# Kernel optimization log

Measured on AMD Instinct MI355X. Metric: run time of the kernel, lower is better.

Reference implementation:

```python
import jax, jax.numpy as jnp
import numpy as np

B, S, HID = 2, 2048, 3072
H, KV, D = 16, 8, 256
EPS = 1e-6
SCALE = D ** -0.5  # query_pre_attn_scalar is None -> head_dim**-0.5
NEG = -1e9


def setup_inputs() -> dict:
    key = jax.random.key(0)
    ks = jax.random.split(key, 7)
    hidden_states = jax.random.normal(ks[0], (B, S, HID), jnp.float32)
    # rotary tables: freqs_cis = exp(i * pos * theta_j), theta_j = 10000^(-2j/D)
    pos = jnp.arange(S, dtype=jnp.float32)
    inv_freq = 1.0 / (10000.0 ** (jnp.arange(0, D, 2, dtype=jnp.float32) / D))  # [D/2]
    ang = pos[:, None] * inv_freq[None, :]  # [S, D/2]
    freqs_cos = jnp.cos(ang)
    freqs_sin = jnp.sin(ang)
    # additive causal mask [1,1,S,S]
    causal = jnp.tril(jnp.ones((S, S), dtype=bool))
    mask = jnp.where(causal, 0.0, NEG).astype(jnp.float32)[None, None]
    q_w = jax.random.normal(ks[1], (HID, H * D), jnp.float32) * 0.02
    k_w = jax.random.normal(ks[2], (HID, KV * D), jnp.float32) * 0.02
    v_w = jax.random.normal(ks[3], (HID, KV * D), jnp.float32) * 0.02
    o_w = jax.random.normal(ks[4], (H * D, HID), jnp.float32) * 0.02
    qnorm_w = jax.random.normal(ks[5], (D,), jnp.float32) * 0.1
    knorm_w = jax.random.normal(ks[6], (D,), jnp.float32) * 0.1
    return dict(hidden_states=hidden_states, freqs_cos=freqs_cos, freqs_sin=freqs_sin,
                mask=mask, q_w=q_w, k_w=k_w, v_w=v_w, o_w=o_w,
                qnorm_w=qnorm_w, knorm_w=knorm_w)


def rmsnorm(x, w, eps=EPS):
    # RMSNorm with add_unit_offset: x * rsqrt(mean(x^2)+eps) * (1 + w)
    x32 = x.astype(jnp.float32)
    n = x32 * jax.lax.rsqrt(jnp.mean(x32 * x32, axis=-1, keepdims=True) + eps)
    return (n * (1.0 + w.astype(jnp.float32))).astype(x.dtype)


def rope(x, cos, sin):
    # x: [B, S, Hx, D]; complex mult with (x1 + i x2), then concat(real, imag)
    x1, x2 = jnp.split(x, 2, axis=-1)  # each [B,S,Hx,D/2]
    c = cos[None, :, None, :]
    s = sin[None, :, None, :]
    return jnp.concatenate([x1 * c - x2 * s, x1 * s + x2 * c], axis=-1)


def reference(hidden_states, freqs_cos, freqs_sin, mask, q_w, k_w, v_w, o_w, qnorm_w, knorm_w):
    bsz, seqlen = hidden_states.shape[0], hidden_states.shape[1]
    xq = (hidden_states @ q_w).reshape(bsz, seqlen, H, D)
    xk = (hidden_states @ k_w).reshape(bsz, seqlen, KV, D)
    xv = (hidden_states @ v_w).reshape(bsz, seqlen, KV, D)
    # QK-norm (use_qk_norm=True)
    xq = rmsnorm(xq, qnorm_w)
    xk = rmsnorm(xk, knorm_w)
    # rotary embeddings
    xq = rope(xq, freqs_cos, freqs_sin)
    xk = rope(xk, freqs_cos, freqs_sin)
    # GQA: repeat kv heads to match query heads
    rep = H // KV
    xk = jnp.repeat(xk, rep, axis=2)
    xv = jnp.repeat(xv, rep, axis=2)
    q = jnp.transpose(xq, (0, 2, 1, 3)) * SCALE  # [B,H,S,D]
    k = jnp.transpose(xk, (0, 2, 1, 3))
    v = jnp.transpose(xv, (0, 2, 1, 3))
    scores = jnp.einsum('bhqd,bhkd->bhqk', q, k) + mask
    probs = jax.nn.softmax(scores.astype(jnp.float32), axis=-1).astype(q.dtype)
    out = jnp.einsum('bhqk,bhkd->bhqd', probs, v)
    out = jnp.transpose(out, (0, 2, 1, 3)).reshape(bsz, seqlen, H * D)
    return out @ o_w
```

## Files before the change

kernel.cpp:

```cpp
#include <hip/hip_runtime.h>
#include <hip/hip_bf16.h>
#include <cstdint>

#define B_   2
#define S_   2048
#define HID_ 3072
#define H_   16
#define KV_  8
#define D_   256
#define HD_  4096
#define KVD_ 2048

constexpr float EPS_   = 1e-6f;
constexpr float SCALE_ = 0.0625f;

typedef unsigned short u16;
typedef __attribute__((ext_vector_type(8))) short bf16x8;
typedef __attribute__((ext_vector_type(4))) float f32x4;

__device__ inline float bf2f(u16 u) { return __uint_as_float(((unsigned int)u) << 16); }
__device__ inline u16 f2bf(float f) {
  unsigned int x = __float_as_uint(f);
  x += 0x7fffu + ((x >> 16) & 1u);
  return (u16)(x >> 16);
}

__device__ inline void gll16(const u16* g, u16* l) {
  __builtin_amdgcn_global_load_lds((const __attribute__((address_space(1))) unsigned int*)g,
                                   (__attribute__((address_space(3))) unsigned int*)l,
                                   16, 0, 0);
}

__global__ void cast_f32_bf16(const float* __restrict__ in, u16* __restrict__ out, int n4) {
  int i = blockIdx.x * blockDim.x + threadIdx.x;
  if (i < n4) {
    float4 v = ((const float4*)in)[i];
    ushort4 o;
    o.x = f2bf(v.x); o.y = f2bf(v.y); o.z = f2bf(v.z); o.w = f2bf(v.w);
    ((ushort4*)out)[i] = o;
  }
}

__global__ void transpose_cast(const float* __restrict__ in, u16* __restrict__ out, int K, int N) {
  __shared__ __align__(16) float tile[64][65];
  int n0 = blockIdx.x * 64, k0 = blockIdx.y * 64;
  int t = threadIdx.x;
  int rr = t >> 4, cc = (t & 15) * 4;
  for (int i = 0; i < 4; i++) {
    float4 v = *(const float4*)(&in[(size_t)(k0 + rr + 16 * i) * N + n0 + cc]);
    tile[rr + 16 * i][cc + 0] = v.x; tile[rr + 16 * i][cc + 1] = v.y;
    tile[rr + 16 * i][cc + 2] = v.z; tile[rr + 16 * i][cc + 3] = v.w;
  }
  __syncthreads();
  for (int i = 0; i < 4; i++) {
    int orow = rr + 16 * i;
    ushort4 o;
    o.x = f2bf(tile[cc + 0][orow]); o.y = f2bf(tile[cc + 1][orow]);
    o.z = f2bf(tile[cc + 2][orow]); o.w = f2bf(tile[cc + 3][orow]);
    *(ushort4*)(&out[(size_t)(n0 + orow) * K + k0 + cc]) = o;
  }
}

__global__ void transpose_v(const u16* __restrict__ in, u16* __restrict__ out) {
  __shared__ __align__(16) u16 tile[64][68];
  int n0 = blockIdx.x * 64, tk0 = blockIdx.y * 64;
  int b = tk0 >> 11, s0 = tk0 & (S_ - 1);
  int t = threadIdx.x;
  int rr = t >> 4, cc = (t & 15) * 4;
  for (int i = 0; i < 4; i++) {
    ushort4 v = *(const ushort4*)(&in[(size_t)(tk0 + rr + 16 * i) * KVD_ + n0 + cc]);
    tile[rr + 16 * i][cc + 0] = v.x; tile[rr + 16 * i][cc + 1] = v.y;
    tile[rr + 16 * i][cc + 2] = v.z; tile[rr + 16 * i][cc + 3] = v.w;
  }
  __syncthreads();
  for (int i = 0; i < 4; i++) {
    int orow = rr + 16 * i;
    ushort4 o;
    o.x = tile[cc + 0][orow]; o.y = tile[cc + 1][orow];
    o.z = tile[cc + 2][orow]; o.w = tile[cc + 3][orow];
    *(ushort4*)(&out[((size_t)b << 22) + (size_t)(n0 + orow) * S_ + s0 + cc]) = o;
  }
}

template <bool OUTF32>
__global__ __launch_bounds__(256) void gemm_bf16(const u16* __restrict__ A,
                                                 const u16* __restrict__ Bt,
                                                 void* __restrict__ Cv, int M, int N, int K) {
  __shared__ __align__(16) u16 As[128 * 32];
  __shared__ __align__(16) u16 Bs[128 * 32];
  int t = threadIdx.x, lane = t & 63, wave = t >> 6;
  int wm = wave >> 1, wn = wave & 1, quad = lane >> 4, l16 = lane & 15;
  int bm = blockIdx.y * 128, bn = blockIdx.x * 128;
  f32x4 acc[4][4] = {};
  int srow = wave * 16 + (lane >> 2);
  int scol = (lane & 3) * 8;
  const u16* ap0 = A  + (size_t)(bm + srow) * K + scol;
  const u16* ap1 = A  + (size_t)(bm + 64 + srow) * K + scol;
  const u16* bp0 = Bt + (size_t)(bn + srow) * K + scol;
  const u16* bp1 = Bt + (size_t)(bn + 64 + srow) * K + scol;
  u16* asb0 = &As[wave * 512];
  u16* asb1 = &As[wave * 512 + 2048];
  u16* bsb0 = &Bs[wave * 512];
  u16* bsb1 = &Bs[wave * 512 + 2048];
  for (int k0 = 0; k0 < K; k0 += 32) {
    __syncthreads();
    gll16(ap0 + k0, asb0);
    gll16(ap1 + k0, asb1);
    gll16(bp0 + k0, bsb0);
    gll16(bp1 + k0, bsb1);
    __syncthreads();
    bf16x8 af[4], bfr[4];
    for (int i = 0; i < 4; i++)
      af[i] = *(const bf16x8*)(&As[(wm * 64 + i * 16 + l16) * 32 + quad * 8]);
    for (int j = 0; j < 4; j++)
      bfr[j] = *(const bf16x8*)(&Bs[(wn * 64 + j * 16 + l16) * 32 + quad * 8]);
    for (int i = 0; i < 4; i++)
      for (int j = 0; j < 4; j++)
        acc[i][j] = __builtin_amdgcn_mfma_f32_16x16x32_bf16(af[i], bfr[j], acc[i][j], 0, 0, 0);
  }
  for (int i = 0; i < 4; i++)
    for (int j = 0; j < 4; j++)
      for (int r = 0; r < 4; r++) {
        int row = bm + wm * 64 + i * 16 + quad * 4 + r;
        int col = bn + wn * 64 + j * 16 + l16;
        float v = acc[i][j][r];
        if (OUTF32) ((float*)Cv)[(size_t)row * N + col] = v;
        else ((u16*)Cv)[(size_t)row * N + col] = f2bf(v);
      }
}

__global__ void rmsnorm_rope(u16* __restrict__ x, const float* __restrict__ w,
                             const float* __restrict__ fc, const float* __restrict__ fsn,
                             int nh, float outscale) {
  int token = blockIdx.x;
  int head = blockIdx.y * 4 + (threadIdx.x >> 6);
  if (head >= nh) return;
  int lane = threadIdx.x & 63;
  int s = token & (S_ - 1);
  u16* p = x + (size_t)(token * nh + head) * D_;
  float v0 = bf2f(p[lane]);
  float v1 = bf2f(p[lane + 64]);
  float v2 = bf2f(p[lane + 128]);
  float v3 = bf2f(p[lane + 192]);
  float ss = v0 * v0 + v1 * v1 + v2 * v2 + v3 * v3;
  for (int off = 32; off; off >>= 1) ss += __shfl_xor(ss, off, 64);
  float rs = rsqrtf(ss * (1.0f / D_) + EPS_);
  float n0 = v0 * rs * (1.0f + w[lane]);
  float n1 = v1 * rs * (1.0f + w[lane + 64]);
  float n2 = v2 * rs * (1.0f + w[lane + 128]);
  float n3 = v3 * rs * (1.0f + w[lane + 192]);
  float c0 = fc[s * 128 + lane], s0 = fsn[s * 128 + lane];
  float c1 = fc[s * 128 + lane + 64], s1 = fsn[s * 128 + lane + 64];
  p[lane]       = f2bf((n0 * c0 - n2 * s0) * outscale);
  p[lane + 128] = f2bf((n0 * s0 + n2 * c0) * outscale);
  p[lane + 64]  = f2bf((n1 * c1 - n3 * s1) * outscale);
  p[lane + 192] = f2bf((n1 * s1 + n3 * c1) * outscale);
}

__global__ __launch_bounds__(256, 3) void flash_attn(const u16* __restrict__ Q,
                                                     const u16* __restrict__ Kb,
                                                     const u16* __restrict__ Vt,
                                                     u16* __restrict__ O) {
  __shared__ __align__(16) u16 Ks[2][8 * 1024];
  __shared__ __align__(16) u16 Vs[8 * 1024];
  int t = threadIdx.x, lane = t & 63, wave = t >> 6;
  int quad = lane >> 4, l16 = lane & 15;
  int h = blockIdx.y, b = blockIdx.z;
  int kvh = h >> 1;

  int swz = ((lane & 3) ^ ((lane >> 2) & 3)) * 8;
  int rswz = (quad ^ (l16 & 3)) * 8;
  const u16* kst = Kb + (size_t)(b * S_ + (lane >> 2)) * KVD_ + kvh * D_ + wave * 64 + swz;
  const u16* vst = Vt + ((size_t)b << 22) + (size_t)(kvh * D_ + wave * 64 + (lane >> 2)) * S_ + swz;

  auto stageK = [&](int kt, int bufi) {
    u16* kdst = &Ks[bufi][wave * 2048];
    const u16* ksrc = kst + (size_t)(kt * 32) * KVD_;
#pragma unroll
    for (int c2 = 0; c2 < 2; c2++)
#pragma unroll
      for (int r = 0; r < 2; r++)
        gll16(ksrc + (size_t)(r * 16) * KVD_ + c2 * 32, kdst + c2 * 1024 + r * 512);
  };
  auto stageV = [&](int kt) {
    u16* vdst = &Vs[wave * 2048];
#pragma unroll
    for (int c = 0; c < 4; c++)
      gll16(vst + (size_t)(c * 16) * S_ + kt * 32, vdst + c * 512);
  };

#pragma unroll 1
  for (int half = 0; half < 2; half++) {
    int qb = (half == 0) ? (31 - (int)blockIdx.x) * 64 : (int)blockIdx.x * 64;
    int qw = qb + wave * 16;

    bf16x8 qf[8];
    const u16* qp = Q + ((size_t)(b * S_) + qw + l16) * HD_ + h * D_;
#pragma unroll
    for (int c = 0; c < 8; c++) qf[c] = *(const bf16x8*)(qp + c * 32 + quad * 8);

    f32x4 o_acc[16] = {};
    float m_s = -3e38f, l_s = 0.f;

    int nkt = (qb + 64) >> 5;
    stageK(0, 0);
    stageV(0);
#pragma unroll 1
    for (int kt = 0; kt < nkt; kt++) {
      int cur = kt & 1;
      asm volatile("s_waitcnt vmcnt(4)" ::: "memory");
      __builtin_amdgcn_s_barrier();
      asm volatile("" ::: "memory");
      if (kt + 1 < nkt) stageK(kt + 1, cur ^ 1);

      f32x4 sc0 = {}, sc1 = {};
#pragma unroll
      for (int c = 0; c < 8; c++) {
        bf16x8 k0 = *(const bf16x8*)(&Ks[cur][c * 1024 + l16 * 32 + rswz]);
        bf16x8 k1 = *(const bf16x8*)(&Ks[cur][c * 1024 + (l16 + 16) * 32 + rswz]);
        sc0 = __builtin_amdgcn_mfma_f32_16x16x32_bf16(k0, qf[c], sc0, 0, 0, 0);
        sc1 = __builtin_amdgcn_mfma_f32_16x16x32_bf16(k1, qf[c], sc1, 0, 0, 0);
      }

      int qg = qw + l16;
      int kbase = kt * 32 + quad * 4;
      float p0[4], p1[4];
      float mx = -1e30f;
#pragma unroll
      for (int r = 0; r < 4; r++) {
        p0[r] = (kbase + r <= qg) ? sc0[r] : -1e30f;
        p1[r] = (kbase + 16 + r <= qg) ? sc1[r] : -1e30f;
        mx = fmaxf(mx, fmaxf(p0[r], p1[r]));
      }
      mx = fmaxf(mx, __shfl_xor(mx, 16));
      mx = fmaxf(mx, __shfl_xor(mx, 32));
      float mn = fmaxf(m_s, mx);
      bool chg = mn > m_s;
      float rsum = 0.f;
#pragma unroll
      for (int r = 0; r < 4; r++) {
        p0[r] = __expf(p0[r] - mn);
        p1[r] = __expf(p1[r] - mn);
        rsum += p0[r] + p1[r];
      }
      if (__any((int)chg)) {
        float alpha = __expf(m_s - mn);
        float ar[4];
#pragma unroll
        for (int r = 0; r < 4; r++) ar[r] = __shfl(alpha, quad * 20 + r);
#pragma unroll
        for (int nt = 0; nt < 16; nt++)
#pragma unroll
          for (int r = 0; r < 4; r++) o_acc[nt][r] *= ar[r];
        l_s *= alpha;
      }
      m_s = mn;
      rsum += __shfl_xor(rsum, 16);
      rsum += __shfl_xor(rsum, 32);
      l_s += rsum;

      unsigned int w_[4], x_[4], gl[4], gh[4], sn[4], rc[4];
      w_[0] = (unsigned)f2bf(p0[0]) | ((unsigned)f2bf(p0[1]) << 16);
      w_[1] = (unsigned)f2bf(p0[2]) | ((unsigned)f2bf(p0[3]) << 16);
      w_[2] = (unsigned)f2bf(p1[0]) | ((unsigned)f2bf(p1[1]) << 16);
      w_[3] = (unsigned)f2bf(p1[2]) | ((unsigned)f2bf(p1[3]) << 16);
#pragma unroll
      for (int i = 0; i < 4; i++) x_[i] = (unsigned)__shfl_xor((int)w_[i], 16);
      bool odd = (quad & 1) != 0;
      gl[0] = odd ? x_[0] : w_[0]; gl[1] = odd ? x_[1] : w_[1];
      gl[2] = odd ? w_[0] : x_[0]; gl[3] = odd ? w_[1] : x_[1];
      gh[0] = odd ? x_[2] : w_[2]; gh[1] = odd ? x_[3] : w_[3];
      gh[2] = odd ? w_[2] : x_[2]; gh[3] = odd ? w_[3] : x_[3];
#pragma unroll
      for (int i = 0; i < 4; i++) sn[i] = odd ? gl[i] : gh[i];
#pragma unroll
      for (int i = 0; i < 4; i++) rc[i] = (unsigned)__shfl_xor((int)sn[i], 32);
      union { unsigned int u[4]; bf16x8 v; } pfc;
#pragma unroll
      for (int i = 0; i < 4; i++)
        pfc.u[i] = (quad == 0) ? gl[i] : (quad == 3) ? gh[i] : rc[i];
      bf16x8 pf = pfc.v;

      if (kt + 1 < nkt) asm volatile("s_waitcnt vmcnt(4)" ::: "memory");
      else              asm volatile("s_waitcnt vmcnt(0)" ::: "memory");
      __builtin_amdgcn_s_barrier();
      asm volatile("" ::: "memory");

#pragma unroll
      for (int nt = 0; nt < 16; nt++) {
        bf16x8 vf = *(const bf16x8*)(&Vs[(nt * 16 + l16) * 32 + rswz]);
        o_acc[nt] = __builtin_amdgcn_mfma_f32_16x16x32_bf16(pf, vf, o_acc[nt], 0, 0, 0);
      }

      asm volatile("s_waitcnt lgkmcnt(0)" ::: "memory");
      __builtin_amdgcn_s_barrier();
      asm volatile("" ::: "memory");
      if (kt + 1 < nkt) stageV(kt + 1);
    }

    float invl = 1.0f / l_s;
    float inv_r[4];
#pragma unroll
    for (int r = 0; r < 4; r++) inv_r[r] = __shfl(invl, quad * 20 + r);
    for (int r = 0; r < 4; r++) {
      int qg2 = qw + quad * 4 + r;
      u16* op = O + ((size_t)(b * S_) + qg2) * HD_ + h * D_;
      for (int nt = 0; nt < 16; nt++) op[nt * 16 + l16] = f2bf(o_acc[nt][r] * inv_r[r]);
    }
  }
}

extern "C" void kernel_launch(void* const* d_in, const int* in_sizes, int n_in,
                              void* d_out, int out_size, void* d_ws, size_t ws_size,
                              hipStream_t stream) {
  const float* hs  = (const float*)d_in[0];
  const float* fc  = (const float*)d_in[1];
  const float* fsn = (const float*)d_in[2];
  const float* qw  = (const float*)d_in[4];
  const float* kw  = (const float*)d_in[5];
  const float* vw  = (const float*)d_in[6];
  const float* ow  = (const float*)d_in[7];
  const float* qnw = (const float*)d_in[8];
  const float* knw = (const float*)d_in[9];

  char* ws = (char*)d_ws;
  u16* x_bf = (u16*)(ws + 0);
  u16* vt   = (u16*)(ws + 0);
  u16* qw_t = (u16*)(ws + 25165824);
  u16* kw_t = (u16*)(ws + 50331648);
  u16* vw_t = (u16*)(ws + 62914560);
  u16* ow_t = (u16*)(ws + 75497472);
  u16* xq   = (u16*)(ws + 100663296);
  u16* xk   = (u16*)(ws + 134217728);
  u16* xv   = (u16*)(ws + 150994944);
  u16* attn = (u16*)(ws + 25165824);

  cast_f32_bf16<<<12288, 256, 0, stream>>>(hs, x_bf, 4096 * 3072 / 4);
  transpose_cast<<<dim3(64, 48), 256, 0, stream>>>(qw, qw_t, 3072, 4096);
  transpose_cast<<<dim3(32, 48), 256, 0, stream>>>(kw, kw_t, 3072, 2048);
  transpose_cast<<<dim3(32, 48), 256, 0, stream>>>(vw, vw_t, 3072, 2048);
  transpose_cast<<<dim3(48, 64), 256, 0, stream>>>(ow, ow_t, 4096, 3072);

  gemm_bf16<false><<<dim3(32, 32), 256, 0, stream>>>(x_bf, qw_t, xq, 4096, 4096, 3072);
  gemm_bf16<false><<<dim3(16, 32), 256, 0, stream>>>(x_bf, kw_t, xk, 4096, 2048, 3072);
  gemm_bf16<false><<<dim3(16, 32), 256, 0, stream>>>(x_bf, vw_t, xv, 4096, 2048, 3072);

  rmsnorm_rope<<<dim3(4096, 4), 256, 0, stream>>>(xq, qnw, fc, fsn, 16, SCALE_);
  rmsnorm_rope<<<dim3(4096, 2), 256, 0, stream>>>(xk, knw, fc, fsn, 8, 1.0f);

  transpose_v<<<dim3(32, 64), 256, 0, stream>>>(xv, vt);

  flash_attn<<<dim3(16, 16, 2), 256, 0, stream>>>(xq, xk, vt, attn);

  gemm_bf16<true><<<dim3(24, 32), 256, 0, stream>>>(attn, ow_t, (float*)d_out, 4096, 3072, 4096);
}
```

Measured before the change: 871.4 us.

## Fuse QKV projections into one 256x256-tile double-buffered GEMM

Replaces the 128x128 single-buffered GEMM with a 256x256-tile, 512-thread kernel. The new kernel double-buffers LDS, swizzles its layout, interleaves MFMA with prefetch under priority hints, and remaps block IDs for L2 locality. The Q, K and V projections become one GEMM over a concatenated weight (q, k, v weights laid out contiguously) that writes an interleaved [tokens, 8192] buffer, and downstream kernels read it with the new stride. This cuts launches, reuses A tiles across all three outputs, and raises MFMA utilization. The risks are higher register and LDS pressure and fewer blocks for the 3072-wide output GEMM (192 blocks).

```diff
diff --git a/kernel.cpp b/kernel.cpp
--- a/kernel.cpp
+++ b/kernel.cpp
@@ -10,6 +10,7 @@
 #define D_   256
 #define HD_  4096
 #define KVD_ 2048
+#define QKS_ 8192
 
 constexpr float EPS_   = 1e-6f;
 constexpr float SCALE_ = 0.0625f;
@@ -68,7 +69,7 @@
   int t = threadIdx.x;
   int rr = t >> 4, cc = (t & 15) * 4;
   for (int i = 0; i < 4; i++) {
-    ushort4 v = *(const ushort4*)(&in[(size_t)(tk0 + rr + 16 * i) * KVD_ + n0 + cc]);
+    ushort4 v = *(const ushort4*)(&in[(size_t)(tk0 + rr + 16 * i) * QKS_ + n0 + cc]);
     tile[rr + 16 * i][cc + 0] = v.x; tile[rr + 16 * i][cc + 1] = v.y;
     tile[rr + 16 * i][cc + 2] = v.z; tile[rr + 16 * i][cc + 3] = v.w;
   }
@@ -83,61 +84,147 @@
 }
 
 template <bool OUTF32>
-__global__ __launch_bounds__(256) void gemm_bf16(const u16* __restrict__ A,
-                                                 const u16* __restrict__ Bt,
-                                                 void* __restrict__ Cv, int M, int N, int K) {
-  __shared__ __align__(16) u16 As[128 * 32];
-  __shared__ __align__(16) u16 Bs[128 * 32];
+__global__ __launch_bounds__(512, 2) void gemm256(const u16* __restrict__ A,
+                                                  const u16* __restrict__ Bt,
+                                                  void* __restrict__ Cv, int M, int N, int K) {
+  __shared__ __align__(16) u16 As[2][16384];
+  __shared__ __align__(16) u16 Bs[2][16384];
   int t = threadIdx.x, lane = t & 63, wave = t >> 6;
-  int wm = wave >> 1, wn = wave & 1, quad = lane >> 4, l16 = lane & 15;
-  int bm = blockIdx.y * 128, bn = blockIdx.x * 128;
-  f32x4 acc[4][4] = {};
-  int srow = wave * 16 + (lane >> 2);
-  int scol = (lane & 3) * 8;
-  const u16* ap0 = A  + (size_t)(bm + srow) * K + scol;
-  const u16* ap1 = A  + (size_t)(bm + 64 + srow) * K + scol;
-  const u16* bp0 = Bt + (size_t)(bn + srow) * K + scol;
-  const u16* bp1 = Bt + (size_t)(bn + 64 + srow) * K + scol;
-  u16* asb0 = &As[wave * 512];
-  u16* asb1 = &As[wave * 512 + 2048];
-  u16* bsb0 = &Bs[wave * 512];
-  u16* bsb1 = &Bs[wave * 512 + 2048];
-  for (int k0 = 0; k0 < K; k0 += 32) {
-    __syncthreads();
-    gll16(ap0 + k0, asb0);
-    gll16(ap1 + k0, asb1);
-    gll16(bp0 + k0, bsb0);
-    gll16(bp1 + k0, bsb1);
-    __syncthreads();
-    bf16x8 af[4], bfr[4];
+  int quad = lane >> 4, l16 = lane & 15;
+  int wm = wave >> 2, wn = wave & 3;
+
+  int nwg = gridDim.x * gridDim.y;
+  int bid = blockIdx.y * gridDim.x + blockIdx.x;
+  int sbid = (bid & 7) * (nwg >> 3) + (bid >> 3);
+  int bn = (sbid % gridDim.x) * 256;
+  int bm = (sbid / gridDim.x) * 256;
+
+  int srow = lane >> 2;
+  int scol8 = ((lane & 3) ^ ((lane >> 3) & 3)) * 8;
+  const u16* ap = A + (size_t)(bm + srow) * K + scol8;
+  const u16* bp = Bt + (size_t)(bn + srow) * K + scol8;
+  int ha1 = (wave & 3) + ((wave >> 2) << 3);
+  int hb1 = (wave & 1) + ((wave >> 1) << 2);
+
+  auto stA = [&](int sr, int sc, int k0, int bufi) {
+    gll16(ap + (size_t)(sr * 16) * K + k0 + sc * 32, &As[bufi][(sr * 2 + sc) * 512]);
+  };
+  auto stB = [&](int sr, int sc, int k0, int bufi) {
+    gll16(bp + (size_t)(sr * 16) * K + k0 + sc * 32, &Bs[bufi][(sr * 2 + sc) * 512]);
+  };
+
+  int rsw = l16 * 32 + ((quad ^ ((l16 >> 1) & 3)) * 8);
+#define LDA8(i, ks) (*(const bf16x8*)(&As[cur][((wm * 8 + (i)) * 2 + (ks)) * 512 + rsw]))
+#define LDB8(j, ks) (*(const bf16x8*)(&Bs[cur][((wn * 4 + (j)) * 2 + (ks)) * 512 + rsw]))
+
+  f32x4 acc[8][4] = {};
+  int NT = K >> 6;
+
+#pragma unroll
+  for (int h = 0; h < 2; h++) {
+    int k0 = h * 64;
+    stA(ha1, 0, k0, h); stA(ha1, 1, k0, h);
+    stA(ha1 + 4, 0, k0, h); stA(ha1 + 4, 1, k0, h);
+    stB(hb1, 0, k0, h); stB(hb1, 1, k0, h);
+    stB(hb1 + 2, 0, k0, h); stB(hb1 + 2, 1, k0, h);
+  }
+  asm volatile("s_waitcnt vmcnt(8)" ::: "memory");
+  __builtin_amdgcn_s_barrier();
+  asm volatile("" ::: "memory");
+
+#pragma unroll 1
+  for (int kt = 0; kt < NT; kt++) {
+    int cur = kt & 1;
+    int kp = (kt + 2) * 64;
+    bool pre = (kt + 2) < NT;
+    bf16x8 a[4][2], b[4][2];
+#pragma unroll
+    for (int i = 0; i < 4; i++) { a[i][0] = LDA8(i, 0); a[i][1] = LDA8(i, 1); }
+#pragma unroll
+    for (int j = 0; j < 2; j++) { b[j][0] = LDB8(j, 0); b[j][1] = LDB8(j, 1); }
+    __builtin_amdgcn_s_barrier();
+    asm volatile("s_waitcnt lgkmcnt(0)" ::: "memory");
+    __builtin_amdgcn_sched_barrier(0);
+    __builtin_amdgcn_s_setprio(1);
+#pragma unroll
     for (int i = 0; i < 4; i++)
-      af[i] = *(const bf16x8*)(&As[(wm * 64 + i * 16 + l16) * 32 + quad * 8]);
+#pragma unroll
+      for (int j = 0; j < 2; j++) {
+        acc[i][j] = __builtin_amdgcn_mfma_f32_16x16x32_bf16(a[i][0], b[j][0], acc[i][j], 0, 0, 0);
+        acc[i][j] = __builtin_amdgcn_mfma_f32_16x16x32_bf16(a[i][1], b[j][1], acc[i][j], 0, 0, 0);
+      }
+    __builtin_amdgcn_s_setprio(0);
+#pragma unroll
+    for (int j = 2; j < 4; j++) { b[j][0] = LDB8(j, 0); b[j][1] = LDB8(j, 1); }
+    if (pre) { stA(ha1, 0, kp, cur); stA(ha1, 1, kp, cur);
+               stB(hb1, 0, kp, cur); stB(hb1, 1, kp, cur); }
+    __builtin_amdgcn_s_barrier();
+    asm volatile("s_waitcnt lgkmcnt(0)" ::: "memory");
+    __builtin_amdgcn_sched_barrier(0);
+    __builtin_amdgcn_s_setprio(1);
+#pragma unroll
+    for (int i = 0; i < 4; i++)
+#pragma unroll
+      for (int j = 2; j < 4; j++) {
+        acc[i][j] = __builtin_amdgcn_mfma_f32_16x16x32_bf16(a[i][0], b[j][0], acc[i][j], 0, 0, 0);
+        acc[i][j] = __builtin_amdgcn_mfma_f32_16x16x32_bf16(a[i][1], b[j][1], acc[i][j], 0, 0, 0);
+      }
+    __builtin_amdgcn_s_setprio(0);
+#pragma unroll
+    for (int i = 0; i < 4; i++) { a[i][0] = LDA8(i + 4, 0); a[i][1] = LDA8(i + 4, 1); }
+    if (pre) { stB(hb1 + 2, 0, kp, cur); stB(hb1 + 2, 1, kp, cur); }
+    __builtin_amdgcn_s_barrier();
+    asm volatile("s_waitcnt lgkmcnt(0)" ::: "memory");
+    __builtin_amdgcn_sched_barrier(0);
+    __builtin_amdgcn_s_setprio(1);
+#pragma unroll
+    for (int i = 0; i < 4; i++)
+#pragma unroll
+      for (int j = 2; j < 4; j++) {
+        acc[i + 4][j] = __builtin_amdgcn_mfma_f32_16x16x32_bf16(a[i][0], b[j][0], acc[i + 4][j], 0, 0, 0);
+        acc[i + 4][j] = __builtin_amdgcn_mfma_f32_16x16x32_bf16(a[i][1], b[j][1], acc[i + 4][j], 0, 0, 0);
+      }
+    __builtin_amdgcn_s_setprio(0);
+    if (pre) { stA(ha1 + 4, 0, kp, cur); stA(ha1 + 4, 1, kp, cur); }
+    __builtin_amdgcn_s_setprio(1);
+#pragma unroll
+    for (int i = 0; i < 4; i++)
+#pragma unroll
+      for (int j = 0; j < 2; j++) {
+        acc[i + 4][j] = __builtin_amdgcn_mfma_f32_16x16x32_bf16(a[i][0], b[j][0], acc[i + 4][j], 0, 0, 0);
+        acc[i + 4][j] = __builtin_amdgcn_mfma_f32_16x16x32_bf16(a[i][1], b[j][1], acc[i + 4][j], 0, 0, 0);
+      }
+    __builtin_amdgcn_s_setprio(0);
+    asm volatile("s_waitcnt vmcnt(8)" ::: "memory");
+    __builtin_amdgcn_s_barrier();
+    asm volatile("" ::: "memory");
+  }
+
+#pragma unroll
+  for (int i = 0; i < 8; i++)
+#pragma unroll
     for (int j = 0; j < 4; j++)
-      bfr[j] = *(const bf16x8*)(&Bs[(wn * 64 + j * 16 + l16) * 32 + quad * 8]);
-    for (int i = 0; i < 4; i++)
-      for (int j = 0; j < 4; j++)
-        acc[i][j] = __builtin_amdgcn_mfma_f32_16x16x32_bf16(af[i], bfr[j], acc[i][j], 0, 0, 0);
-  }
-  for (int i = 0; i < 4; i++)
-    for (int j = 0; j < 4; j++)
+#pragma unroll
       for (int r = 0; r < 4; r++) {
-        int row = bm + wm * 64 + i * 16 + quad * 4 + r;
+        int row = bm + wm * 128 + i * 16 + quad * 4 + r;
         int col = bn + wn * 64 + j * 16 + l16;
         float v = acc[i][j][r];
         if (OUTF32) ((float*)Cv)[(size_t)row * N + col] = v;
         else ((u16*)Cv)[(size_t)row * N + col] = f2bf(v);
       }
+#undef LDA8
+#undef LDB8
 }
 
 __global__ void rmsnorm_rope(u16* __restrict__ x, const float* __restrict__ w,
                              const float* __restrict__ fc, const float* __restrict__ fsn,
-                             int nh, float outscale) {
+                             int nh, int stride, float outscale) {
   int token = blockIdx.x;
   int head = blockIdx.y * 4 + (threadIdx.x >> 6);
   if (head >= nh) return;
   int lane = threadIdx.x & 63;
   int s = token & (S_ - 1);
-  u16* p = x + (size_t)(token * nh + head) * D_;
+  u16* p = x + (size_t)token * stride + head * D_;
   float v0 = bf2f(p[lane]);
   float v1 = bf2f(p[lane + 64]);
   float v2 = bf2f(p[lane + 128]);
@@ -170,17 +257,17 @@
 
   int swz = ((lane & 3) ^ ((lane >> 2) & 3)) * 8;
   int rswz = (quad ^ (l16 & 3)) * 8;
-  const u16* kst = Kb + (size_t)(b * S_ + (lane >> 2)) * KVD_ + kvh * D_ + wave * 64 + swz;
+  const u16* kst = Kb + (size_t)(b * S_ + (lane >> 2)) * QKS_ + kvh * D_ + wave * 64 + swz;
   const u16* vst = Vt + ((size_t)b << 22) + (size_t)(kvh * D_ + wave * 64 + (lane >> 2)) * S_ + swz;
 
   auto stageK = [&](int kt, int bufi) {
     u16* kdst = &Ks[bufi][wave * 2048];
-    const u16* ksrc = kst + (size_t)(kt * 32) * KVD_;
+    const u16* ksrc = kst + (size_t)(kt * 32) * QKS_;
 #pragma unroll
     for (int c2 = 0; c2 < 2; c2++)
 #pragma unroll
       for (int r = 0; r < 2; r++)
-        gll16(ksrc + (size_t)(r * 16) * KVD_ + c2 * 32, kdst + c2 * 1024 + r * 512);
+        gll16(ksrc + (size_t)(r * 16) * QKS_ + c2 * 32, kdst + c2 * 1024 + r * 512);
   };
   auto stageV = [&](int kt) {
     u16* vdst = &Vs[wave * 2048];
@@ -195,7 +282,7 @@
     int qw = qb + wave * 16;
 
     bf16x8 qf[8];
-    const u16* qp = Q + ((size_t)(b * S_) + qw + l16) * HD_ + h * D_;
+    const u16* qp = Q + ((size_t)(b * S_) + qw + l16) * QKS_ + h * D_;
 #pragma unroll
     for (int c = 0; c < 8; c++) qf[c] = *(const bf16x8*)(qp + c * 32 + quad * 8);
 
@@ -324,33 +411,29 @@
   const float* knw = (const float*)d_in[9];
 
   char* ws = (char*)d_ws;
-  u16* x_bf = (u16*)(ws + 0);
-  u16* vt   = (u16*)(ws + 0);
-  u16* qw_t = (u16*)(ws + 25165824);
-  u16* kw_t = (u16*)(ws + 50331648);
-  u16* vw_t = (u16*)(ws + 62914560);
-  u16* ow_t = (u16*)(ws + 75497472);
-  u16* xq   = (u16*)(ws + 100663296);
-  u16* xk   = (u16*)(ws + 134217728);
-  u16* xv   = (u16*)(ws + 150994944);
-  u16* attn = (u16*)(ws + 25165824);
+  u16* x_bf   = (u16*)(ws + 0);
+  u16* vt     = (u16*)(ws + 0);
+  u16* wqkv_t = (u16*)(ws + 25165824);
+  u16* kw_t   = (u16*)(ws + 50331648);
+  u16* vw_t   = (u16*)(ws + 62914560);
+  u16* ow_t   = (u16*)(ws + 75497472);
+  u16* xqkv   = (u16*)(ws + 100663296);
+  u16* attn   = (u16*)(ws + 25165824);
 
   cast_f32_bf16<<<12288, 256, 0, stream>>>(hs, x_bf, 4096 * 3072 / 4);
-  transpose_cast<<<dim3(64, 48), 256, 0, stream>>>(qw, qw_t, 3072, 4096);
+  transpose_cast<<<dim3(64, 48), 256, 0, stream>>>(qw, wqkv_t, 3072, 4096);
   transpose_cast<<<dim3(32, 48), 256, 0, stream>>>(kw, kw_t, 3072, 2048);
   transpose_cast<<<dim3(32, 48), 256, 0, stream>>>(vw, vw_t, 3072, 2048);
   transpose_cast<<<dim3(48, 64), 256, 0, stream>>>(ow, ow_t, 4096, 3072);
 
-  gemm_bf16<false><<<dim3(32, 32), 256, 0, stream>>>(x_bf, qw_t, xq, 4096, 4096, 3072);
-  gemm_bf16<false><<<dim3(16, 32), 256, 0, stream>>>(x_bf, kw_t, xk, 4096, 2048, 3072);
-  gemm_bf16<false><<<dim3(16, 32), 256, 0, stream>>>(x_bf, vw_t, xv, 4096, 2048, 3072);
-
-  rmsnorm_rope<<<dim3(4096, 4), 256, 0, stream>>>(xq, qnw, fc, fsn, 16, SCALE_);
-  rmsnorm_rope<<<dim3(4096, 2), 256, 0, stream>>>(xk, knw, fc, fsn, 8, 1.0f);
-
-  transpose_v<<<dim3(32, 64), 256, 0, stream>>>(xv, vt);
-
-  flash_attn<<<dim3(16, 16, 2), 256, 0, stream>>>(xq, xk, vt, attn);
-
-  gemm_bf16<true><<<dim3(24, 32), 256, 0, stream>>>(attn, ow_t, (float*)d_out, 4096, 3072, 4096);
-}
+  gemm256<false><<<dim3(32, 16), 512, 0, stream>>>(x_bf, wqkv_t, xqkv, 4096, 8192, 3072);
+
+  rmsnorm_rope<<<dim3(4096, 4), 256, 0, stream>>>(xqkv, qnw, fc, fsn, 16, QKS_, SCALE_);
+  rmsnorm_rope<<<dim3(4096, 2), 256, 0, stream>>>(xqkv + 4096, knw, fc, fsn, 8, QKS_, 1.0f);
+
+  transpose_v<<<dim3(32, 64), 256, 0, stream>>>(xqkv + 6144, vt);
+
+  flash_attn<<<dim3(16, 16, 2), 256, 0, stream>>>(xqkv, xqkv + 4096, vt, attn);
+
+  gemm256<true><<<dim3(12, 16), 512, 0, stream>>>(attn, ow_t, (float*)d_out, 4096, 3072, 4096);
+}
```

Result: faster. 769.5 us (-11.7%).
